# Performance work log

Measured on AMD Instinct MI355X. Metric: run time of the kernel, lower is better.

## Reference

```python
import jax, jax.numpy as jnp
import numpy as np

EPS = 1e-3  # nn.LayerNorm(eps=0.001)
PADDING = 0.0


def setup_inputs() -> dict:
    key = jax.random.key(0)
    k1, k2, k3, k4 = jax.random.split(key, 4)
    N, M, K3, C_IN, C_OUT, B = 200000, 40000, 27, 64, 128, 4
    features = jax.random.normal(k1, (N, C_IN), dtype=jnp.float32)
    center_coors = jax.random.normal(k2, (M, 3), dtype=jnp.float32)
    voxel_idx = jax.random.randint(k3, (M, K3), 0, N, dtype=jnp.int64)
    num_list = jnp.full((B,), M // B, dtype=jnp.int32)
    W = jax.random.normal(k4, (K3 * C_IN, C_OUT), dtype=jnp.float32) * 1e-4
    gamma = jnp.ones((C_OUT,), dtype=jnp.float32)
    beta = jnp.zeros((C_OUT,), dtype=jnp.float32)
    return {
        "features": features,
        "center_coors": center_coors,
        "voxel_idx": voxel_idx,
        "num_list": num_list,
        "W": W,
        "gamma": gamma,
        "beta": beta,
        "num_keypoints": 2048,
    }


def _block(features, voxel_idx, W, gamma, beta):
    M, K3 = voxel_idx.shape
    C_in = features.shape[1]
    # voxel neighbor gather; negative idx -> padding value
    gathered = features[jnp.clip(voxel_idx, 0, features.shape[0] - 1)]  # [M, K3, C_in]
    gathered = jnp.where(voxel_idx[..., None] < 0, PADDING, gathered)
    flat = gathered.reshape(M, K3 * C_in)
    out = flat @ W  # [M, C_out]
    # LayerNorm over channel dim (per-batch loop in torch is mathematically
    # identical to a single row-wise LayerNorm)
    mu = jnp.mean(out, axis=-1, keepdims=True)
    var = jnp.mean(jnp.square(out - mu), axis=-1, keepdims=True)
    out = (out - mu) / jnp.sqrt(var + EPS) * gamma + beta
    return jax.nn.relu(out)


def _resample(out_features, center_coors, num_list, num_keypoints):
    B = num_list.shape[0]
    K = num_keypoints
    accum = jnp.cumsum(num_list)
    offsets = jnp.concatenate([jnp.zeros((1,), accum.dtype), accum[:-1]])  # [B]
    j = jnp.arange(K, dtype=jnp.int32)  # [K]
    end = jnp.minimum(num_list, jnp.int32(K))  # [B]
    valid = j[None, :] < end[:, None]  # [B, K]
    src = jnp.clip(offsets[:, None] + j[None, :], 0, out_features.shape[0] - 1)  # [B, K]
    res_feat = jnp.where(valid[..., None], out_features[src], 0.0)  # [B, K, C]
    res_xyz = jnp.where(valid[..., None], center_coors[src], 0.0)  # [B, K, 3]
    # replicate original quirk: segments 0..B-2 get batch index 1..B-1, last stays 0
    bid = jnp.arange(B, dtype=jnp.float32)
    col0 = jnp.where(bid < B - 1, bid + 1.0, 0.0)  # [B]
    col0 = jnp.broadcast_to(col0[:, None, None], (B, K, 1))
    res_coor = jnp.concatenate([col0, res_xyz], axis=-1)  # [B, K, 4]
    C = out_features.shape[1]
    return res_feat.reshape(B * K, C), res_coor.reshape(B * K, 4)


def reference(features, center_coors, voxel_idx, num_list, W, gamma, beta, num_keypoints):
    out = _block(features, voxel_idx, W, gamma, beta)
    point_features, point_coords = _resample(out, center_coors, num_list, num_keypoints)
    return point_features, point_coords
```

## Files before the change

kernel.cpp:

```cpp
#include <hip/hip_runtime.h>
#include <hip/hip_bf16.h>
#include <stdint.h>
#include <stddef.h>

#define TM 16
#define CIN 64
#define NK3 27
#define NK3P 28
#define COUT 128
#define EPS_LN 1e-3f
#define KCH  (NK3 * CIN / 32)
#define KCHP (NK3P * CIN / 32)
#define NT   (COUT / 16)
#define NPAIR (NK3P / 2)
#define PK_BYTES (NT * KCHP * 64 * 8 * 2)

typedef __attribute__((ext_vector_type(8))) short   short8;
typedef __attribute__((ext_vector_type(4))) float   floatx4;
typedef __attribute__((ext_vector_type(4))) unsigned short ushort4v;

__device__ __forceinline__ unsigned short f2b(float f) {
    union { float f; unsigned int i; } v;
    v.f = f;
    unsigned int i = v.i;
    return (unsigned short)((i + 0x7fffu + ((i >> 16) & 1u)) >> 16);
}

__global__ __launch_bounds__(256) void pack_w(const float* __restrict__ Wm,
                                              const int* __restrict__ voxel_idx,
                                              const int* __restrict__ num_list,
                                              int Bc,
                                              unsigned short* __restrict__ pk,
                                              int* __restrict__ flags) {
    const int t = threadIdx.x;
    if (blockIdx.x == 0 && t < 64) {
        int wv = voxel_idx[2 * t + 1];
        unsigned long long nz = __ballot(wv != 0);
        if (t == 0) {
            int f = (nz == 0ULL) ? 1 : 0;
            bool n64 = false;
            if (Bc >= 2) {
                n64 = (num_list[1] == 0) && (num_list[0] != 0);
                if (Bc >= 4) n64 = n64 && (num_list[3] == 0);
            }
            if (n64) f |= 2;
            flags[0] = f;
        }
    }
    int slot = blockIdx.x * 256 + t;
    int l  = slot & 63;
    int kk = (slot >> 6) % KCHP;
    int nt = slot / (64 * KCHP);
    short8 v = {0, 0, 0, 0, 0, 0, 0, 0};
    if (kk < KCH) {
        int q = l >> 4, n = l & 15;
        const float* src = Wm + (size_t)(kk * 32 + q * 8) * COUT + nt * 16 + n;
        #pragma unroll
        for (int j = 0; j < 8; ++j)
            v[j] = (short)f2b(src[(size_t)j * COUT]);
    }
    *(short8*)(pk + (size_t)slot * 8) = v;
}

__global__ __launch_bounds__(512) void dpc_mfma(
    const float* __restrict__ features,
    const float* __restrict__ center,
    const int* __restrict__ voxel_idx,
    const int* __restrict__ num_list,
    const unsigned short* __restrict__ pk,
    const int* __restrict__ flags,
    const float* __restrict__ gamma_,
    const float* __restrict__ beta_,
    float* __restrict__ out_feat,
    float* __restrict__ out_coor,
    int N, int M, int B, int K, int Rtot)
{
    __shared__ int s_vid[TM][NK3P];
    __shared__ int s_src[TM];
    __shared__ int s_valid[TM];
    __shared__ __align__(16) unsigned short s_a[3][2048];
    __shared__ float s_c[TM][COUT + 4];

    const int t  = threadIdx.x;
    const int R0 = blockIdx.x * TM;

    const int fl = flags[0];
    const bool vidx64 = (fl & 1) != 0;
    const bool nl64   = (fl & 2) != 0;

    if (t < TM) {
        int r = R0 + t;
        int src = 0, valid = 0;
        if (r < Rtot) {
            int b = r / K;
            int j = r - b * K;
            int offs = 0, nlb = 0;
            for (int i = 0; i < B; ++i) {
                int v = nl64 ? num_list[2 * i] : num_list[i];
                if (i < b) offs += v;
                if (i == b) nlb = v;
            }
            int end = nlb < K ? nlb : K;
            valid = (j < end) ? 1 : 0;
            src = offs + j;
            if (src < 0) src = 0;
            if (src > M - 1) src = M - 1;
        }
        s_src[t] = src;
        s_valid[t] = valid;
    }
    __syncthreads();

    if (t < TM * 4) {
        int i = t >> 2, comp = t & 3;
        int r = R0 + i;
        if (r < Rtot) {
            float val;
            if (comp == 0) {
                int b = r / K;
                val = (b < B - 1) ? (float)(b + 1) : 0.0f;
            } else {
                val = s_valid[i] ? center[(size_t)s_src[i] * 3 + comp - 1] : 0.0f;
            }
            out_coor[(size_t)r * 4 + comp] = val;
        }
    }

    for (int lin = t; lin < TM * NK3P; lin += 512) {
        int i = lin / NK3P;
        int k = lin - i * NK3P;
        int v = -1;
        if (k < NK3) {
            size_t e = (size_t)s_src[i] * NK3 + k;
            v = vidx64 ? voxel_idx[2 * e] : voxel_idx[e];
        }
        s_vid[i][k] = v;
    }
    __syncthreads();

    const int sub = t >> 8;
    const int rem = t & 255;
    const int m   = rem >> 4;
    const int c0  = (rem & 15) * 4;
    const int chunk = c0 >> 5;
    const int q4    = (c0 & 31) >> 3;
    const int j0    = c0 & 7;
    const int aoff  = sub * 1024 + chunk * 512 + (q4 * 16 + m) * 8 + j0;

    auto gatherPair = [&](int p) -> float4 {
        int idx = s_vid[m][2 * p + sub];
        float4 r = make_float4(0.f, 0.f, 0.f, 0.f);
        if (idx >= 0) {
            if (idx > N - 1) idx = N - 1;
            r = *(const float4*)(features + (size_t)idx * CIN + c0);
        }
        return r;
    };
    auto stash = [&](int buf, float4 v) {
        ushort4v u;
        u[0] = f2b(v.x); u[1] = f2b(v.y); u[2] = f2b(v.z); u[3] = f2b(v.w);
        *(ushort4v*)&s_a[buf][aoff] = u;
    };

    const int w    = t >> 6;
    const int lane = t & 63;
    auto loadB = [&](int kk) -> short8 {
        return *(const short8*)(pk + ((size_t)(w * KCHP + kk) * 64 + lane) * 8);
    };

    floatx4 acc = {0.f, 0.f, 0.f, 0.f};

    stash(0, gatherPair(0));
    float4 cA = gatherPair(1);
    short8 bb0 = loadB(0), bb1 = loadB(1), bb2 = loadB(2), bb3 = loadB(3);
    __syncthreads();

    for (int p = 0; p < NPAIR; ++p) {
        const bool hasC = (p + 1 < NPAIR);
        const bool hasN = (p + 2 < NPAIR);

        float4 nA;
        if (hasN) nA = gatherPair(p + 2);
        short8 nb0, nb1, nb2, nb3;
        if (hasC) {
            const int kk = 4 * (p + 1);
            nb0 = loadB(kk); nb1 = loadB(kk + 1); nb2 = loadB(kk + 2); nb3 = loadB(kk + 3);
        }

        const int buf = p % 3;
        const short8 a0 = *(const short8*)&s_a[buf][       lane * 8];
        const short8 a1 = *(const short8*)&s_a[buf][ 512 + lane * 8];
        const short8 a2 = *(const short8*)&s_a[buf][1024 + lane * 8];
        const short8 a3 = *(const short8*)&s_a[buf][1536 + lane * 8];

        acc = __builtin_amdgcn_mfma_f32_16x16x32_bf16(a0, bb0, acc, 0, 0, 0);
        acc = __builtin_amdgcn_mfma_f32_16x16x32_bf16(a1, bb1, acc, 0, 0, 0);
        acc = __builtin_amdgcn_mfma_f32_16x16x32_bf16(a2, bb2, acc, 0, 0, 0);
        acc = __builtin_amdgcn_mfma_f32_16x16x32_bf16(a3, bb3, acc, 0, 0, 0);

        if (hasC) stash((p + 1) % 3, cA);
        __syncthreads();
        if (hasC) { bb0 = nb0; bb1 = nb1; bb2 = nb2; bb3 = nb3; }
        if (hasN) cA = nA;
    }

    {
        const int cq = lane >> 4, n = lane & 15;
        #pragma unroll
        for (int reg = 0; reg < 4; ++reg)
            s_c[cq * 4 + reg][w * 16 + n] = acc[reg];
    }
    __syncthreads();

    const int c2 = lane * 2;
    const float g0  = gamma_[c2];
    const float g1  = gamma_[c2 + 1];
    const float be0 = beta_[c2];
    const float be1 = beta_[c2 + 1];

    #pragma unroll
    for (int i = 0; i < 2; ++i) {
        int row = w * 2 + i;
        float a0 = s_c[row][c2];
        float a1 = s_c[row][c2 + 1];
        float s  = a0 + a1;
        float ss = a0 * a0 + a1 * a1;
        #pragma unroll
        for (int mm = 1; mm < 64; mm <<= 1) {
            s  += __shfl_xor(s,  mm, 64);
            ss += __shfl_xor(ss, mm, 64);
        }
        float mu   = s * (1.0f / COUT);
        float var  = ss * (1.0f / COUT) - mu * mu;
        float rstd = rsqrtf(var + EPS_LN);
        float v0 = (a0 - mu) * rstd * g0 + be0;
        float v1 = (a1 - mu) * rstd * g1 + be1;
        v0 = fmaxf(v0, 0.f);
        v1 = fmaxf(v1, 0.f);
        if (!s_valid[row]) { v0 = 0.f; v1 = 0.f; }
        int r = R0 + row;
        if (r < Rtot) {
            out_feat[(size_t)r * COUT + c2]     = v0;
            out_feat[(size_t)r * COUT + c2 + 1] = v1;
        }
    }
}

extern "C" void kernel_launch(void* const* d_in, const int* in_sizes, int n_in,
                              void* d_out, int out_size, void* d_ws, size_t ws_size,
                              hipStream_t stream) {
    const float* features = (const float*)d_in[0];
    const float* center   = (const float*)d_in[1];
    const int*   vidx     = (const int*)d_in[2];
    const int*   num_list = (const int*)d_in[3];
    const float* Wm       = (const float*)d_in[4];
    const float* gamma_   = (const float*)d_in[5];
    const float* beta_    = (const float*)d_in[6];

    const int B    = in_sizes[3];
    const int Cout = in_sizes[5];
    const int M    = in_sizes[1] / 3;
    const int K3v  = in_sizes[2] / M;
    const int Cin  = (in_sizes[4] / Cout) / K3v;
    const int N    = in_sizes[0] / Cin;
    const int Rtot = out_size / (Cout + 4);
    const int K    = Rtot / B;

    float* out_feat = (float*)d_out;
    float* out_coor = out_feat + (size_t)Rtot * Cout;

    unsigned short* pk = (unsigned short*)d_ws;
    int* flags = (int*)((char*)d_ws + PK_BYTES);

    const int pack_grid = (NT * KCHP * 64) / 256;
    pack_w<<<dim3(pack_grid), dim3(256), 0, stream>>>(Wm, vidx, num_list, B, pk, flags);

    const int tiles = (Rtot + TM - 1) / TM;
    dpc_mfma<<<dim3(tiles), dim3(512), 0, stream>>>(
        features, center, vidx, num_list, pk, flags, gamma_, beta_,
        out_feat, out_coor, N, M, B, K, Rtot);
}
```

Baseline: 110.4 us.

## Gather all neighbor features into LDS upfront, drop per-step barriers

Replaces the triple-buffered, barrier-per-step gather/MFMA pipeline with one bulk gather phase. All 28 neighbor slices of the A tile are loaded into LDS, seven gathers in flight per thread per batch, with a single barrier before the MFMA loop. This removes 14 __syncthreads and exposes more memory-level parallelism for the random feature gathers. In exchange, LDS use grows to about 56KB per block, which can cap occupancy, and it adds a launch-bounds occupancy hint of 4.

```diff
diff --git a/kernel.cpp b/kernel.cpp
--- a/kernel.cpp
+++ b/kernel.cpp
@@ -62,7 +62,7 @@
     *(short8*)(pk + (size_t)slot * 8) = v;
 }
 
-__global__ __launch_bounds__(512) void dpc_mfma(
+__global__ __launch_bounds__(512, 4) void dpc_mfma(
     const float* __restrict__ features,
     const float* __restrict__ center,
     const int* __restrict__ voxel_idx,
@@ -78,7 +78,7 @@
     __shared__ int s_vid[TM][NK3P];
     __shared__ int s_src[TM];
     __shared__ int s_valid[TM];
-    __shared__ __align__(16) unsigned short s_a[3][2048];
+    __shared__ __align__(16) unsigned short s_a[NK3P * 1024];
     __shared__ float s_c[TM][COUT + 4];
 
     const int t  = threadIdx.x;
@@ -145,10 +145,10 @@
     const int chunk = c0 >> 5;
     const int q4    = (c0 & 31) >> 3;
     const int j0    = c0 & 7;
-    const int aoff  = sub * 1024 + chunk * 512 + (q4 * 16 + m) * 8 + j0;
-
-    auto gatherPair = [&](int p) -> float4 {
-        int idx = s_vid[m][2 * p + sub];
+    const int abase = chunk * 512 + (q4 * 16 + m) * 8 + j0;
+
+    auto gatherKc = [&](int kc) -> float4 {
+        int idx = s_vid[m][kc];
         float4 r = make_float4(0.f, 0.f, 0.f, 0.f);
         if (idx >= 0) {
             if (idx > N - 1) idx = N - 1;
@@ -156,11 +156,28 @@
         }
         return r;
     };
-    auto stash = [&](int buf, float4 v) {
+    auto stashKc = [&](int kc, float4 v) {
         ushort4v u;
         u[0] = f2b(v.x); u[1] = f2b(v.y); u[2] = f2b(v.z); u[3] = f2b(v.w);
-        *(ushort4v*)&s_a[buf][aoff] = u;
+        *(ushort4v*)&s_a[kc * 1024 + abase] = u;
     };
+
+    {
+        float4 g0_, g1_, g2_, g3_, g4_, g5_, g6_;
+        g0_ = gatherKc(sub);      g1_ = gatherKc(2 + sub);  g2_ = gatherKc(4 + sub);
+        g3_ = gatherKc(6 + sub);  g4_ = gatherKc(8 + sub);  g5_ = gatherKc(10 + sub);
+        g6_ = gatherKc(12 + sub);
+        stashKc(sub, g0_);        stashKc(2 + sub, g1_);    stashKc(4 + sub, g2_);
+        stashKc(6 + sub, g3_);    stashKc(8 + sub, g4_);    stashKc(10 + sub, g5_);
+        stashKc(12 + sub, g6_);
+        g0_ = gatherKc(14 + sub); g1_ = gatherKc(16 + sub); g2_ = gatherKc(18 + sub);
+        g3_ = gatherKc(20 + sub); g4_ = gatherKc(22 + sub); g5_ = gatherKc(24 + sub);
+        g6_ = gatherKc(26 + sub);
+        stashKc(14 + sub, g0_);   stashKc(16 + sub, g1_);   stashKc(18 + sub, g2_);
+        stashKc(20 + sub, g3_);   stashKc(22 + sub, g4_);   stashKc(24 + sub, g5_);
+        stashKc(26 + sub, g6_);
+    }
+    __syncthreads();
 
     const int w    = t >> 6;
     const int lane = t & 63;
@@ -169,39 +186,27 @@
     };
 
     floatx4 acc = {0.f, 0.f, 0.f, 0.f};
-
-    stash(0, gatherPair(0));
-    float4 cA = gatherPair(1);
     short8 bb0 = loadB(0), bb1 = loadB(1), bb2 = loadB(2), bb3 = loadB(3);
-    __syncthreads();
 
     for (int p = 0; p < NPAIR; ++p) {
-        const bool hasC = (p + 1 < NPAIR);
-        const bool hasN = (p + 2 < NPAIR);
-
-        float4 nA;
-        if (hasN) nA = gatherPair(p + 2);
         short8 nb0, nb1, nb2, nb3;
-        if (hasC) {
+        const bool hn = (p + 1 < NPAIR);
+        if (hn) {
             const int kk = 4 * (p + 1);
             nb0 = loadB(kk); nb1 = loadB(kk + 1); nb2 = loadB(kk + 2); nb3 = loadB(kk + 3);
         }
-
-        const int buf = p % 3;
-        const short8 a0 = *(const short8*)&s_a[buf][       lane * 8];
-        const short8 a1 = *(const short8*)&s_a[buf][ 512 + lane * 8];
-        const short8 a2 = *(const short8*)&s_a[buf][1024 + lane * 8];
-        const short8 a3 = *(const short8*)&s_a[buf][1536 + lane * 8];
+        const int base = p * 2048;
+        const short8 a0 = *(const short8*)&s_a[base +        lane * 8];
+        const short8 a1 = *(const short8*)&s_a[base +  512 + lane * 8];
+        const short8 a2 = *(const short8*)&s_a[base + 1024 + lane * 8];
+        const short8 a3 = *(const short8*)&s_a[base + 1536 + lane * 8];
 
         acc = __builtin_amdgcn_mfma_f32_16x16x32_bf16(a0, bb0, acc, 0, 0, 0);
         acc = __builtin_amdgcn_mfma_f32_16x16x32_bf16(a1, bb1, acc, 0, 0, 0);
         acc = __builtin_amdgcn_mfma_f32_16x16x32_bf16(a2, bb2, acc, 0, 0, 0);
         acc = __builtin_amdgcn_mfma_f32_16x16x32_bf16(a3, bb3, acc, 0, 0, 0);
 
-        if (hasC) stash((p + 1) % 3, cA);
-        __syncthreads();
-        if (hasC) { bb0 = nb0; bb1 = nb1; bb2 = nb2; bb3 = nb3; }
-        if (hasN) cA = nA;
+        if (hn) { bb0 = nb0; bb1 = nb1; bb2 = nb2; bb3 = nb3; }
     }
 
     {
```

Measured after the change: 110.9 us. About the same (+0.4%).
